# Kernel optimization log

Measured on AMD Instinct MI355X. Metric: run time of the kernel, lower is better.

The kernel has to match this reference:

```python
import jax, jax.numpy as jnp
import numpy as np
from jax import lax

N, CIN, H, W = 128, 1024, 14, 14
CF, TH = 128, 128          # cv_filter, te_hidden
HP, GT, FP, A = 256, 256, 256, 32


def setup_inputs() -> dict:
    key = jax.random.key(0)
    ks = jax.random.split(key, 12)
    s = 0.05
    return {
        "image": jax.random.normal(ks[0], (N, CIN, H, W), jnp.float32),
        "code": jax.random.normal(ks[1], (N, TH), jnp.float32),
        "conv_w": jax.random.normal(ks[2], (CF, CIN, 3, 3), jnp.float32) * 0.02,
        "conv_b": jnp.zeros((CF,), jnp.float32),
        "hp_w0": jax.random.normal(ks[3], (CF + 2 + TH, HP), jnp.float32) * s,
        "hp_b0": jnp.zeros((HP,), jnp.float32),
        "hp_w1": jax.random.normal(ks[4], (HP, 1), jnp.float32) * s,
        "hp_b1": jnp.zeros((1,), jnp.float32),
        "gt_w0": jax.random.normal(ks[5], ((CF + 2) * 2 + TH, GT), jnp.float32) * s,
        "gt_b0": jnp.zeros((GT,), jnp.float32),
        "gt_w1": jax.random.normal(ks[6], (GT, GT), jnp.float32) * s,
        "gt_b1": jnp.zeros((GT,), jnp.float32),
        "fp_w0": jax.random.normal(ks[7], (GT, FP), jnp.float32) * s,
        "fp_b0": jnp.zeros((FP,), jnp.float32),
        "fp_w1": jax.random.normal(ks[8], (FP, A), jnp.float32) * s,
        "fp_b1": jnp.zeros((A,), jnp.float32),
    }


def _sarn(image, code, conv_w, conv_b, hp_w0, hp_b0, hp_w1, hp_b1,
          gt_w0, gt_b0, gt_w1, gt_b1, fp_w0, fp_b0, fp_w1, fp_b1):
    # visual_resize: 3x3 conv, stride 1, pad 1 (NCHW)
    x = lax.conv_general_dilated(image, conv_w, (1, 1), "SAME",
                                 dimension_numbers=("NCHW", "OIHW", "NCHW"))
    x = x + conv_b[None, :, None, None]                       # [n, cf, h, w]
    n, c, h, w = x.shape
    o = h * w
    # sarn_encode: append x/y coordinate channels and question code
    xc = jnp.broadcast_to(jnp.linspace(-1.0, 1.0, h).reshape(1, 1, h, 1), (n, 1, h, w))
    yc = jnp.broadcast_to(jnp.linspace(-1.0, 1.0, w).reshape(1, 1, 1, w), (n, 1, h, w))
    coord = jnp.concatenate([x, xc, yc], axis=1)              # [n, cf+2, h, w]
    q = jnp.broadcast_to(code[:, :, None, None], (n, code.shape[1], h, w))
    qenc = jnp.concatenate([coord, q], axis=1)                # [n, cf+2+th, h, w]
    ce = coord.reshape(n, c + 2, o).transpose(0, 2, 1)        # [n, o, cf+2]
    qe = qenc.reshape(n, -1, o).transpose(0, 2, 1)            # [n, o, cf+2+th]
    # h_psi: per-object attention logit
    a = jax.nn.relu(jnp.einsum("nod,dh->noh", qe, hp_w0) + hp_b0)
    att = jnp.einsum("noh,hk->nok", a, hp_w1) + hp_b1         # [n, o, 1]
    # sarn_pair: softmax select a single soft object, pair with every object
    sel = jax.nn.softmax(att[..., 0], axis=1)                 # [n, o]
    selected = jnp.einsum("no,nod->nd", sel, ce)              # [n, cf+2]
    pairs = jnp.concatenate(
        [qe, jnp.broadcast_to(selected[:, None, :], ce.shape)], axis=2)  # [n, o, 2*(cf+2)+th]
    # g_theta MLP + sum over objects
    g = jax.nn.relu(jnp.einsum("nop,pg->nog", pairs, gt_w0) + gt_b0)
    g = jax.nn.relu(jnp.einsum("nog,gk->nok", g, gt_w1) + gt_b1)
    relations = g.sum(axis=1)                                 # [n, gt]
    # f_phi MLP -> answer logits
    f = jax.nn.relu(relations @ fp_w0 + fp_b0)
    return f @ fp_w1 + fp_b1                                  # [n, a_size]


def reference(image, code, conv_w, conv_b, hp_w0, hp_b0, hp_w1, hp_b1,
              gt_w0, gt_b0, gt_w1, gt_b1, fp_w0, fp_b0, fp_w1, fp_b1):
    return _sarn(image, code, conv_w, conv_b, hp_w0, hp_b0, hp_w1, hp_b1,
                 gt_w0, gt_b0, gt_w1, gt_b1, fp_w0, fp_b0, fp_w1, fp_b1)
```

## Files before the change

### kernel.cpp

```cpp
#include <hip/hip_runtime.h>
#include <stdint.h>

typedef unsigned short u16;
typedef __bf16 bf16x8 __attribute__((ext_vector_type(8)));
typedef float f32x4 __attribute__((ext_vector_type(4)));

__device__ __forceinline__ u16 f2b(float f) {
  union { float f; uint32_t u; } v; v.f = f;
  uint32_t r = v.u + 0x7fffu + ((v.u >> 16) & 1u);
  return (u16)(r >> 16);
}
__device__ __forceinline__ float b2f(u16 b) {
  union { float f; uint32_t u; } v; v.u = ((uint32_t)b) << 16;
  return v.f;
}
__device__ __forceinline__ void g2l16(const void* g, void* l) {
  __builtin_amdgcn_global_load_lds(
      (const __attribute__((address_space(1))) void*)g,
      (__attribute__((address_space(3))) void*)l, 16, 0, 0);
}

#define N_SAMP 128
#define OPAD   224
#define ROWS   (N_SAMP * OPAD)

__global__ __launch_bounds__(256) void prep_weights(
    const float* __restrict__ conv_w, const float* __restrict__ hp_w0,
    const float* __restrict__ gt_w0, const float* __restrict__ gt_w1,
    u16* __restrict__ W2, u16* __restrict__ hp_w0t,
    u16* __restrict__ gt_w0t, u16* __restrict__ gt_w1t) {
  int idx = blockIdx.x * 256 + threadIdx.x;
  const int nW2 = 9 * 128 * 1024;
  const int nHP = 256 * 288;
  const int nGT0 = 256 * 288;
  const int nGT1 = 256 * 256;
  if (idx < nW2) {
    int s = idx / 131072; int r = idx & 131071;
    int cf = r >> 10; int cin = r & 1023;
    W2[idx] = f2b(conv_w[(cf * 1024 + cin) * 9 + s]);
    return;
  }
  idx -= nW2;
  if (idx < nHP) {
    int nn = idx / 288, kk = idx % 288;
    hp_w0t[nn * 288 + kk] = (kk < 258) ? f2b(hp_w0[kk * 256 + nn]) : (u16)0;
    return;
  }
  idx -= nHP;
  if (idx < nGT0) {
    int nn = idx / 288, kk = idx % 288;
    gt_w0t[nn * 288 + kk] = (kk < 258) ? f2b(gt_w0[kk * 256 + nn]) : (u16)0;
    return;
  }
  idx -= nGT0;
  if (idx < nGT1) {
    int nn = idx >> 8, kk = idx & 255;
    gt_w1t[nn * 256 + kk] = f2b(gt_w1[kk * 256 + nn]);
  }
}

__global__ __launch_bounds__(256) void prep_img(const float* __restrict__ image,
                                                u16* __restrict__ imgT) {
  __shared__ float t[64][197];
  int n = blockIdx.x >> 4;
  int cin0 = (blockIdx.x & 15) * 64;
  const float* src = image + ((size_t)n * 1024 + cin0) * 196;
  for (int e = threadIdx.x; e < 64 * 196; e += 256) {
    int c = e / 196, sp = e % 196;
    t[c][sp] = src[c * 196 + sp];
  }
  __syncthreads();
  int w = threadIdx.x >> 6, lane = threadIdx.x & 63;
  for (int i = 0; i < 64; ++i) {
    int spg = i * 4 + w;
    int gy = spg >> 4, gx = spg & 15;
    float v = 0.f;
    if (gy >= 1 && gy <= 14 && gx >= 1 && gx <= 14) v = t[lane][(gy - 1) * 14 + (gx - 1)];
    imgT[(((size_t)(n * 256 + spg)) << 10) + cin0 + lane] = f2b(v);
  }
}

__global__ __launch_bounds__(256) void fill_qe(const float* __restrict__ code,
                                               u16* __restrict__ qeb) {
  int base = blockIdx.x * 8;
  for (int rr = 0; rr < 8; ++rr) {
    int r = base + rr;
    int n = r / 224, o = r % 224;
    int y = o / 14, x = o % 14;
    bool valid = o < 196;
    u16* row = qeb + (size_t)r * 288;
    for (int c = threadIdx.x; c < 288; c += 256) {
      u16 v;
      if (c < 128) { if (valid) continue; v = 0; }
      else if (c == 128) v = valid ? f2b(-1.f + 2.f * y / 13.f) : (u16)0;
      else if (c == 129) v = valid ? f2b(-1.f + 2.f * x / 13.f) : (u16)0;
      else if (c < 258) v = valid ? f2b(code[n * 128 + (c - 130)]) : (u16)0;
      else v = 0;
      row[c] = v;
    }
  }
}

__global__ __launch_bounds__(256) void conv_gemm(
    const u16* __restrict__ imgT, const u16* __restrict__ W2,
    const float* __restrict__ conv_b, u16* __restrict__ qeb) {
  __shared__ __align__(16) u16 lA[112 * 32];
  __shared__ __align__(16) u16 lB[128 * 32];
  int tid = threadIdx.x, lane = tid & 63, w = tid >> 6;
  int wg = blockIdx.x;
  int n = wg >> 1;
  int oBase = (wg & 1) * 112;
  int kb = (lane & 3) * 8;

  int oA0 = oBase + w * 16 + (lane >> 2);
  int oA1 = oBase + (w + 4) * 16 + (lane >> 2);
  int y0 = oA0 / 14, x0 = oA0 % 14; bool v0 = oA0 < 196;
  int y1 = oA1 / 14, x1 = oA1 % 14; bool v1 = oA1 < 196;
  bool has1 = (w < 3);

  int cf0 = w * 16 + (lane >> 2);
  int cf1 = (w + 4) * 16 + (lane >> 2);

  f32x4 acc[7][2];
#pragma unroll
  for (int mt = 0; mt < 7; ++mt)
#pragma unroll
    for (int j = 0; j < 2; ++j) acc[mt][j] = (f32x4){0.f, 0.f, 0.f, 0.f};

  int colW = w * 32;
  for (int s = 0; s < 9; ++s) {
    int dy = s / 3, dx = s % 3;
    int sp0 = v0 ? ((y0 + dy) * 16 + (x0 + dx)) : 0;
    int sp1 = v1 ? ((y1 + dy) * 16 + (x1 + dx)) : 0;
    const u16* gA0 = imgT + (((size_t)(n * 256 + sp0)) << 10) + kb;
    const u16* gA1 = imgT + (((size_t)(n * 256 + sp1)) << 10) + kb;
    const u16* gB0 = W2 + (((size_t)(s * 128 + cf0)) << 10) + kb;
    const u16* gB1 = W2 + (((size_t)(s * 128 + cf1)) << 10) + kb;
    for (int cb = 0; cb < 32; ++cb) {
      __syncthreads();
      g2l16(gA0 + cb * 32, &lA[w * 512]);
      if (has1) g2l16(gA1 + cb * 32, &lA[(w + 4) * 512]);
      g2l16(gB0 + cb * 32, &lB[w * 512]);
      g2l16(gB1 + cb * 32, &lB[(w + 4) * 512]);
      __syncthreads();
      bf16x8 af[7];
#pragma unroll
      for (int mt = 0; mt < 7; ++mt)
        af[mt] = *(const bf16x8*)&lA[(mt * 16 + (lane & 15)) * 32 + (lane >> 4) * 8];
#pragma unroll
      for (int j = 0; j < 2; ++j) {
        bf16x8 bfr = *(const bf16x8*)&lB[(colW + j * 16 + (lane & 15)) * 32 + (lane >> 4) * 8];
#pragma unroll
        for (int mt = 0; mt < 7; ++mt)
          acc[mt][j] = __builtin_amdgcn_mfma_f32_16x16x32_bf16(af[mt], bfr, acc[mt][j], 0, 0, 0);
      }
    }
  }
  int q = lane >> 4, c = lane & 15;
#pragma unroll
  for (int mt = 0; mt < 7; ++mt)
#pragma unroll
    for (int j = 0; j < 2; ++j) {
      int cf = colW + j * 16 + c;
      float bv = conv_b[cf];
#pragma unroll
      for (int r = 0; r < 4; ++r) {
        int o = oBase + mt * 16 + q * 4 + r;
        if (o < 196) qeb[(size_t)(n * 224 + o) * 288 + cf] = f2b(acc[mt][j][r] + bv);
      }
    }
}

template <int MODE, int KP, int KC>
__global__ __launch_bounds__(256) void gemm_kernel(
    const u16* __restrict__ A, const u16* __restrict__ Bt,
    const float* __restrict__ bias, const float* __restrict__ vec,
    float* __restrict__ outF, u16* __restrict__ outB) {
  __shared__ __align__(16) u16 lA[112 * 32];
  __shared__ __align__(16) u16 lB[128 * 32];
  int tid = threadIdx.x, lane = tid & 63, w = tid >> 6;
  int bx = blockIdx.x, by = blockIdx.y;
  int r0 = bx * 112;
  int cBase = by * 128;
  int kb = (lane & 3) * 8;
  int rA0 = r0 + w * 16 + (lane >> 2);
  int rA1 = r0 + (w + 4) * 16 + (lane >> 2);
  bool has1 = (w < 3);
  const u16* gA0 = A + (size_t)rA0 * KP + kb;
  const u16* gA1 = A + (size_t)rA1 * KP + kb;
  int cB0 = cBase + w * 16 + (lane >> 2);
  int cB1 = cBase + (w + 4) * 16 + (lane >> 2);
  const u16* gB0 = Bt + (size_t)cB0 * KP + kb;
  const u16* gB1 = Bt + (size_t)cB1 * KP + kb;

  f32x4 acc[7][2];
#pragma unroll
  for (int mt = 0; mt < 7; ++mt)
#pragma unroll
    for (int j = 0; j < 2; ++j) acc[mt][j] = (f32x4){0.f, 0.f, 0.f, 0.f};
  int colW = w * 32;

  for (int cb = 0; cb < KC; ++cb) {
    __syncthreads();
    g2l16(gA0 + cb * 32, &lA[w * 512]);
    if (has1) g2l16(gA1 + cb * 32, &lA[(w + 4) * 512]);
    g2l16(gB0 + cb * 32, &lB[w * 512]);
    g2l16(gB1 + cb * 32, &lB[(w + 4) * 512]);
    __syncthreads();
    bf16x8 af[7];
#pragma unroll
    for (int mt = 0; mt < 7; ++mt)
      af[mt] = *(const bf16x8*)&lA[(mt * 16 + (lane & 15)) * 32 + (lane >> 4) * 8];
#pragma unroll
    for (int j = 0; j < 2; ++j) {
      bf16x8 bfr = *(const bf16x8*)&lB[(colW + j * 16 + (lane & 15)) * 32 + (lane >> 4) * 8];
#pragma unroll
      for (int mt = 0; mt < 7; ++mt)
        acc[mt][j] = __builtin_amdgcn_mfma_f32_16x16x32_bf16(af[mt], bfr, acc[mt][j], 0, 0, 0);
    }
  }

  int q = lane >> 4, c = lane & 15;
  if (MODE == 0) {
    float attp[7][4];
#pragma unroll
    for (int mt = 0; mt < 7; ++mt)
#pragma unroll
      for (int r = 0; r < 4; ++r) attp[mt][r] = 0.f;
#pragma unroll
    for (int j = 0; j < 2; ++j) {
      int col = cBase + colW + j * 16 + c;
      float b0 = bias[col], w1 = vec[col];
#pragma unroll
      for (int mt = 0; mt < 7; ++mt)
#pragma unroll
        for (int r = 0; r < 4; ++r) {
          float v = fmaxf(acc[mt][j][r] + b0, 0.f);
          attp[mt][r] += v * w1;
        }
    }
#pragma unroll
    for (int mt = 0; mt < 7; ++mt)
#pragma unroll
      for (int r = 0; r < 4; ++r) {
        float p = attp[mt][r];
        p += __shfl_xor(p, 1, 64);
        p += __shfl_xor(p, 2, 64);
        p += __shfl_xor(p, 4, 64);
        p += __shfl_xor(p, 8, 64);
        if (c == 0) atomicAdd(&outF[r0 + mt * 16 + q * 4 + r], p);
      }
  } else if (MODE == 1) {
    int n = bx >> 1;
#pragma unroll
    for (int mt = 0; mt < 7; ++mt)
#pragma unroll
      for (int j = 0; j < 2; ++j) {
        int col = cBase + colW + j * 16 + c;
        float b = bias[n * 256 + col];
#pragma unroll
        for (int r = 0; r < 4; ++r) {
          int row = r0 + mt * 16 + q * 4 + r;
          outB[(size_t)row * 256 + col] = f2b(fmaxf(acc[mt][j][r] + b, 0.f));
        }
      }
  } else {
    int n = bx >> 1;
    int ob = (bx & 1) * 112;
#pragma unroll
    for (int j = 0; j < 2; ++j) {
      int col = cBase + colW + j * 16 + c;
      float b = bias[col];
      float sum = 0.f;
#pragma unroll
      for (int mt = 0; mt < 7; ++mt)
#pragma unroll
        for (int r = 0; r < 4; ++r) {
          int o = ob + mt * 16 + q * 4 + r;
          if (o < 196) sum += fmaxf(acc[mt][j][r] + b, 0.f);
        }
      sum += __shfl_xor(sum, 16, 64);
      sum += __shfl_xor(sum, 32, 64);
      if (q == 0) atomicAdd(&outF[n * 256 + col], sum);
    }
  }
}

__global__ __launch_bounds__(256) void sel_kernel(
    const float* __restrict__ att, const u16* __restrict__ qeb,
    const float* __restrict__ gt_w0, const float* __restrict__ gt_b0,
    float* __restrict__ bias2) {
  int n = blockIdx.x, t = threadIdx.x;
  __shared__ float sm[196];
  __shared__ float sel[130];
  __shared__ float red[8];
  float a = (t < 196) ? att[n * 224 + t] : -1e30f;
  float m = a;
  for (int mask = 1; mask < 64; mask <<= 1) m = fmaxf(m, __shfl_xor(m, mask, 64));
  if ((t & 63) == 0) red[t >> 6] = m;
  __syncthreads();
  float M = fmaxf(fmaxf(red[0], red[1]), fmaxf(red[2], red[3]));
  float e = (t < 196) ? expf(a - M) : 0.f;
  float sAcc = e;
  for (int mask = 1; mask < 64; mask <<= 1) sAcc += __shfl_xor(sAcc, mask, 64);
  if ((t & 63) == 0) red[4 + (t >> 6)] = sAcc;
  __syncthreads();
  float S = red[4] + red[5] + red[6] + red[7];
  if (t < 196) sm[t] = e / S;
  __syncthreads();
  if (t < 130) {
    float acc = 0.f;
    const u16* col = qeb + (size_t)n * 224 * 288 + t;
    for (int o = 0; o < 196; ++o) acc += sm[o] * b2f(col[(size_t)o * 288]);
    sel[t] = acc;
  }
  __syncthreads();
  float acc2 = gt_b0[t];
  for (int d = 0; d < 130; ++d) acc2 += sel[d] * gt_w0[(258 + d) * 256 + t];
  bias2[n * 256 + t] = acc2;
}

__global__ __launch_bounds__(256) void fphi(
    const float* __restrict__ relations, const float* __restrict__ fp_w0,
    const float* __restrict__ fp_b0, const float* __restrict__ fp_w1,
    const float* __restrict__ fp_b1, float* __restrict__ out) {
  int n = blockIdx.x, t = threadIdx.x;
  __shared__ float rel[256];
  __shared__ float f[256];
  rel[t] = relations[n * 256 + t];
  __syncthreads();
  float acc = fp_b0[t];
  for (int k = 0; k < 256; ++k) acc += rel[k] * fp_w0[k * 256 + t];
  f[t] = fmaxf(acc, 0.f);
  __syncthreads();
  if (t < 32) {
    float o = fp_b1[0];
    for (int k = 0; k < 256; ++k) o += f[k] * fp_w1[k * 32 + t];
    out[n * 32 + t] = o;
  }
}

extern "C" void kernel_launch(void* const* d_in, const int* in_sizes, int n_in,
                              void* d_out, int out_size, void* d_ws, size_t ws_size,
                              hipStream_t stream) {
  const float* image = (const float*)d_in[0];
  const float* code = (const float*)d_in[1];
  const float* conv_w = (const float*)d_in[2];
  const float* conv_b = (const float*)d_in[3];
  const float* hp_w0 = (const float*)d_in[4];
  const float* hp_b0 = (const float*)d_in[5];
  const float* hp_w1 = (const float*)d_in[6];
  const float* gt_w0 = (const float*)d_in[8];
  const float* gt_b0 = (const float*)d_in[9];
  const float* gt_w1 = (const float*)d_in[10];
  const float* gt_b1 = (const float*)d_in[11];
  const float* fp_w0 = (const float*)d_in[12];
  const float* fp_b0 = (const float*)d_in[13];
  const float* fp_w1 = (const float*)d_in[14];
  const float* fp_b1 = (const float*)d_in[15];
  float* out = (float*)d_out;

  char* p = (char*)d_ws;
  u16* imgT = (u16*)p;   p += (size_t)128 * 256 * 1024 * 2;
  u16* W2 = (u16*)p;     p += (size_t)9 * 128 * 1024 * 2;
  u16* qeb = (u16*)p;    p += (size_t)ROWS * 288 * 2;
  u16* hp_w0t = (u16*)p; p += (size_t)256 * 288 * 2;
  u16* gt_w0t = (u16*)p; p += (size_t)256 * 288 * 2;
  u16* gt_w1t = (u16*)p; p += (size_t)256 * 256 * 2;
  float* att = (float*)p;   p += (size_t)ROWS * 4;
  float* bias2 = (float*)p; p += (size_t)128 * 256 * 4;
  u16* g1 = (u16*)p;        p += (size_t)ROWS * 256 * 2;
  float* relations = (float*)p; p += (size_t)128 * 256 * 4;

  hipMemsetAsync(att, 0, (size_t)ROWS * 4, stream);
  hipMemsetAsync(relations, 0, (size_t)128 * 256 * 4, stream);

  prep_weights<<<5440, 256, 0, stream>>>(conv_w, hp_w0, gt_w0, gt_w1, W2, hp_w0t, gt_w0t, gt_w1t);
  prep_img<<<2048, 256, 0, stream>>>(image, imgT);
  fill_qe<<<ROWS / 8, 256, 0, stream>>>(code, qeb);
  conv_gemm<<<256, 256, 0, stream>>>(imgT, W2, conv_b, qeb);
  gemm_kernel<0, 288, 9><<<dim3(256, 2), 256, 0, stream>>>(qeb, hp_w0t, hp_b0, hp_w1, att, nullptr);
  sel_kernel<<<128, 256, 0, stream>>>(att, qeb, gt_w0, gt_b0, bias2);
  gemm_kernel<1, 288, 9><<<dim3(256, 2), 256, 0, stream>>>(qeb, gt_w0t, bias2, nullptr, nullptr, g1);
  gemm_kernel<2, 256, 8><<<dim3(256, 2), 256, 0, stream>>>(g1, gt_w1t, gt_b1, nullptr, relations, nullptr);
  fphi<<<128, 256, 0, stream>>>(relations, fp_w0, fp_b0, fp_w1, fp_b1, out);
}
```

Baseline: 459.1 us.

## Split conv GEMM over kernel rows with atomic reduction and swizzled LDS

The conv GEMM is split three ways along the 3x3 kernel taps, with 768 blocks in an XCD-aware ordering instead of 256. Partial sums are accumulated by fp32 atomics into a new buffer, and a separate conv_fix kernel adds the bias and writes bf16. The K-tile grows to 64, and XOR-swizzled LDS layouts are added to the conv and the generic GEMMs to avoid bank conflicts. sel_kernel now stages the qeb columns in shared memory before its strided reduction. The cost is an extra memset, extra atomics traffic and one more launch, with the g1 buffer aliased onto convAcc.

```diff
diff --git a/kernel.cpp b/kernel.cpp
--- a/kernel.cpp
+++ b/kernel.cpp
@@ -103,23 +103,28 @@
 
 __global__ __launch_bounds__(256) void conv_gemm(
     const u16* __restrict__ imgT, const u16* __restrict__ W2,
-    const float* __restrict__ conv_b, u16* __restrict__ qeb) {
-  __shared__ __align__(16) u16 lA[112 * 32];
-  __shared__ __align__(16) u16 lB[128 * 32];
+    float* __restrict__ convAcc) {
+  __shared__ __align__(16) u16 lA[112 * 64];
+  __shared__ __align__(16) u16 lB[128 * 64];
   int tid = threadIdx.x, lane = tid & 63, w = tid >> 6;
   int wg = blockIdx.x;
-  int n = wg >> 1;
-  int oBase = (wg & 1) * 112;
-  int kb = (lane & 3) * 8;
-
-  int oA0 = oBase + w * 16 + (lane >> 2);
-  int oA1 = oBase + (w + 4) * 16 + (lane >> 2);
-  int y0 = oA0 / 14, x0 = oA0 % 14; bool v0 = oA0 < 196;
-  int y1 = oA1 / 14, x1 = oA1 % 14; bool v1 = oA1 < 196;
-  bool has1 = (w < 3);
-
-  int cf0 = w * 16 + (lane >> 2);
-  int cf1 = (w + 4) * 16 + (lane >> 2);
+  int xcd = wg & 7, grp = wg >> 3;
+  int n = ((grp / 6) << 3) | xcd;
+  int r6 = grp % 6;
+  int oh = r6 / 3, ks = r6 % 3;
+  int oBase = oh * 112;
+  size_t nBase = (size_t)n << 8;
+  int rowIn = lane >> 3;
+  int cA = ((lane & 7) ^ rowIn) << 3;
+
+  int yxA[4];
+  for (int ii = 0; ii < 4; ++ii) {
+    int t = w + ii * 4;
+    int o = oBase + t * 8 + rowIn;
+    bool valid = o < 196;
+    int y = o / 14, x = o - y * 14;
+    yxA[ii] = valid ? (y * 16 + x) : 0;
+  }
 
   f32x4 acc[7][2];
 #pragma unroll
@@ -127,48 +132,70 @@
 #pragma unroll
     for (int j = 0; j < 2; ++j) acc[mt][j] = (f32x4){0.f, 0.f, 0.f, 0.f};
 
-  int colW = w * 32;
-  for (int s = 0; s < 9; ++s) {
-    int dy = s / 3, dx = s % 3;
-    int sp0 = v0 ? ((y0 + dy) * 16 + (x0 + dx)) : 0;
-    int sp1 = v1 ? ((y1 + dy) * 16 + (x1 + dx)) : 0;
-    const u16* gA0 = imgT + (((size_t)(n * 256 + sp0)) << 10) + kb;
-    const u16* gA1 = imgT + (((size_t)(n * 256 + sp1)) << 10) + kb;
-    const u16* gB0 = W2 + (((size_t)(s * 128 + cf0)) << 10) + kb;
-    const u16* gB1 = W2 + (((size_t)(s * 128 + cf1)) << 10) + kb;
-    for (int cb = 0; cb < 32; ++cb) {
+  int l = lane & 15, q = lane >> 4;
+  for (int si = 0; si < 3; ++si) {
+    int s = ks * 3 + si;
+    int off = (s / 3) * 16 + (s % 3);
+    const u16* Ws = W2 + ((size_t)(s * 128) << 10);
+    for (int cb = 0; cb < 16; ++cb) {
+      int k0 = cb << 6;
       __syncthreads();
-      g2l16(gA0 + cb * 32, &lA[w * 512]);
-      if (has1) g2l16(gA1 + cb * 32, &lA[(w + 4) * 512]);
-      g2l16(gB0 + cb * 32, &lB[w * 512]);
-      g2l16(gB1 + cb * 32, &lB[(w + 4) * 512]);
+      g2l16(imgT + ((nBase + (size_t)(yxA[0] + off)) << 10) + k0 + cA, &lA[(w) * 512]);
+      g2l16(imgT + ((nBase + (size_t)(yxA[1] + off)) << 10) + k0 + cA, &lA[(w + 4) * 512]);
+      g2l16(imgT + ((nBase + (size_t)(yxA[2] + off)) << 10) + k0 + cA, &lA[(w + 8) * 512]);
+      if (w < 2)
+        g2l16(imgT + ((nBase + (size_t)(yxA[3] + off)) << 10) + k0 + cA, &lA[(w + 12) * 512]);
+#pragma unroll
+      for (int ii = 0; ii < 4; ++ii) {
+        int t = w + ii * 4;
+        g2l16(Ws + ((size_t)(t * 8 + rowIn) << 10) + k0 + cA, &lB[t * 512]);
+      }
       __syncthreads();
-      bf16x8 af[7];
-#pragma unroll
-      for (int mt = 0; mt < 7; ++mt)
-        af[mt] = *(const bf16x8*)&lA[(mt * 16 + (lane & 15)) * 32 + (lane >> 4) * 8];
-#pragma unroll
-      for (int j = 0; j < 2; ++j) {
-        bf16x8 bfr = *(const bf16x8*)&lB[(colW + j * 16 + (lane & 15)) * 32 + (lane >> 4) * 8];
+#pragma unroll
+      for (int kk = 0; kk < 2; ++kk) {
+        int co = ((((kk << 2) | q) ^ (l & 7)) << 3);
+        bf16x8 af[7];
 #pragma unroll
         for (int mt = 0; mt < 7; ++mt)
-          acc[mt][j] = __builtin_amdgcn_mfma_f32_16x16x32_bf16(af[mt], bfr, acc[mt][j], 0, 0, 0);
+          af[mt] = *(const bf16x8*)&lA[(mt * 16 + l) * 64 + co];
+#pragma unroll
+        for (int jj = 0; jj < 2; ++jj) {
+          bf16x8 bb = *(const bf16x8*)&lB[(w * 32 + jj * 16 + l) * 64 + co];
+#pragma unroll
+          for (int mt = 0; mt < 7; ++mt)
+            acc[mt][jj] = __builtin_amdgcn_mfma_f32_16x16x32_bf16(af[mt], bb, acc[mt][jj], 0, 0, 0);
+        }
       }
     }
   }
-  int q = lane >> 4, c = lane & 15;
-#pragma unroll
-  for (int mt = 0; mt < 7; ++mt)
-#pragma unroll
-    for (int j = 0; j < 2; ++j) {
-      int cf = colW + j * 16 + c;
-      float bv = conv_b[cf];
-#pragma unroll
-      for (int r = 0; r < 4; ++r) {
-        int o = oBase + mt * 16 + q * 4 + r;
-        if (o < 196) qeb[(size_t)(n * 224 + o) * 288 + cf] = f2b(acc[mt][j][r] + bv);
+#pragma unroll
+  for (int mt = 0; mt < 7; ++mt) {
+    int o = oBase + mt * 16 + q * 4;
+#pragma unroll
+    for (int r4 = 0; r4 < 4; ++r4) {
+      if (o + r4 < 196) {
+        float* dst = convAcc + (size_t)(n * 224 + o + r4) * 128 + w * 32 + l;
+        atomicAdd(dst, acc[mt][0][r4]);
+        atomicAdd(dst + 16, acc[mt][1][r4]);
       }
     }
+  }
+}
+
+__global__ __launch_bounds__(256) void conv_fix(
+    const float* __restrict__ convAcc, const float* __restrict__ conv_b,
+    u16* __restrict__ qeb) {
+  int idx = blockIdx.x * 256 + threadIdx.x;
+  int row196 = idx >> 5;
+  int c0 = (idx & 31) << 2;
+  int n = row196 / 196, o = row196 - n * 196;
+  size_t row = (size_t)(n * 224 + o);
+  const float4 v = *(const float4*)(convAcc + (row << 7) + c0);
+  const float4 b = *(const float4*)(conv_b + c0);
+  ushort4 pk;
+  pk.x = f2b(v.x + b.x); pk.y = f2b(v.y + b.y);
+  pk.z = f2b(v.z + b.z); pk.w = f2b(v.w + b.w);
+  *(ushort4*)(qeb + row * 288 + c0) = pk;
 }
 
 template <int MODE, int KP, int KC>
@@ -182,7 +209,7 @@
   int bx = blockIdx.x, by = blockIdx.y;
   int r0 = bx * 112;
   int cBase = by * 128;
-  int kb = (lane & 3) * 8;
+  int kb = (((lane & 3) ^ ((lane >> 3) & 3)) << 3);
   int rA0 = r0 + w * 16 + (lane >> 2);
   int rA1 = r0 + (w + 4) * 16 + (lane >> 2);
   bool has1 = (w < 3);
@@ -199,6 +226,8 @@
 #pragma unroll
     for (int j = 0; j < 2; ++j) acc[mt][j] = (f32x4){0.f, 0.f, 0.f, 0.f};
   int colW = w * 32;
+  int l = lane & 15, q = lane >> 4;
+  int co = ((q ^ ((l >> 1) & 3)) << 3);
 
   for (int cb = 0; cb < KC; ++cb) {
     __syncthreads();
@@ -210,17 +239,17 @@
     bf16x8 af[7];
 #pragma unroll
     for (int mt = 0; mt < 7; ++mt)
-      af[mt] = *(const bf16x8*)&lA[(mt * 16 + (lane & 15)) * 32 + (lane >> 4) * 8];
+      af[mt] = *(const bf16x8*)&lA[(mt * 16 + l) * 32 + co];
 #pragma unroll
     for (int j = 0; j < 2; ++j) {
-      bf16x8 bfr = *(const bf16x8*)&lB[(colW + j * 16 + (lane & 15)) * 32 + (lane >> 4) * 8];
+      bf16x8 bfr = *(const bf16x8*)&lB[(colW + j * 16 + l) * 32 + co];
 #pragma unroll
       for (int mt = 0; mt < 7; ++mt)
         acc[mt][j] = __builtin_amdgcn_mfma_f32_16x16x32_bf16(af[mt], bfr, acc[mt][j], 0, 0, 0);
     }
   }
 
-  int q = lane >> 4, c = lane & 15;
+  int q4 = lane >> 4, c = lane & 15;
   if (MODE == 0) {
     float attp[7][4];
 #pragma unroll
@@ -248,7 +277,7 @@
         p += __shfl_xor(p, 2, 64);
         p += __shfl_xor(p, 4, 64);
         p += __shfl_xor(p, 8, 64);
-        if (c == 0) atomicAdd(&outF[r0 + mt * 16 + q * 4 + r], p);
+        if (c == 0) atomicAdd(&outF[r0 + mt * 16 + q4 * 4 + r], p);
       }
   } else if (MODE == 1) {
     int n = bx >> 1;
@@ -260,7 +289,7 @@
         float b = bias[n * 256 + col];
 #pragma unroll
         for (int r = 0; r < 4; ++r) {
-          int row = r0 + mt * 16 + q * 4 + r;
+          int row = r0 + mt * 16 + q4 * 4 + r;
           outB[(size_t)row * 256 + col] = f2b(fmaxf(acc[mt][j][r] + b, 0.f));
         }
       }
@@ -276,12 +305,12 @@
       for (int mt = 0; mt < 7; ++mt)
 #pragma unroll
         for (int r = 0; r < 4; ++r) {
-          int o = ob + mt * 16 + q * 4 + r;
+          int o = ob + mt * 16 + q4 * 4 + r;
           if (o < 196) sum += fmaxf(acc[mt][j][r] + b, 0.f);
         }
       sum += __shfl_xor(sum, 16, 64);
       sum += __shfl_xor(sum, 32, 64);
-      if (q == 0) atomicAdd(&outF[n * 256 + col], sum);
+      if (q4 == 0) atomicAdd(&outF[n * 256 + col], sum);
     }
   }
 }
@@ -291,27 +320,33 @@
     const float* __restrict__ gt_w0, const float* __restrict__ gt_b0,
     float* __restrict__ bias2) {
   int n = blockIdx.x, t = threadIdx.x;
+  int w = t >> 6, lane = t & 63;
+  __shared__ u16 sq[196][130];
   __shared__ float sm[196];
   __shared__ float sel[130];
   __shared__ float red[8];
+  const u16* base = qeb + (size_t)n * 224 * 288;
+  for (int o = w; o < 196; o += 4) {
+    const u16* rowp = base + (size_t)o * 288;
+    for (int c = lane; c < 130; c += 64) sq[o][c] = rowp[c];
+  }
   float a = (t < 196) ? att[n * 224 + t] : -1e30f;
   float m = a;
   for (int mask = 1; mask < 64; mask <<= 1) m = fmaxf(m, __shfl_xor(m, mask, 64));
-  if ((t & 63) == 0) red[t >> 6] = m;
+  if (lane == 0) red[w] = m;
   __syncthreads();
   float M = fmaxf(fmaxf(red[0], red[1]), fmaxf(red[2], red[3]));
   float e = (t < 196) ? expf(a - M) : 0.f;
   float sAcc = e;
   for (int mask = 1; mask < 64; mask <<= 1) sAcc += __shfl_xor(sAcc, mask, 64);
-  if ((t & 63) == 0) red[4 + (t >> 6)] = sAcc;
+  if (lane == 0) red[4 + w] = sAcc;
   __syncthreads();
   float S = red[4] + red[5] + red[6] + red[7];
   if (t < 196) sm[t] = e / S;
   __syncthreads();
   if (t < 130) {
     float acc = 0.f;
-    const u16* col = qeb + (size_t)n * 224 * 288 + t;
-    for (int o = 0; o < 196; ++o) acc += sm[o] * b2f(col[(size_t)o * 288]);
+    for (int o = 0; o < 196; ++o) acc += sm[o] * b2f(sq[o][t]);
     sel[t] = acc;
   }
   __syncthreads();
@@ -369,16 +404,19 @@
   u16* gt_w1t = (u16*)p; p += (size_t)256 * 256 * 2;
   float* att = (float*)p;   p += (size_t)ROWS * 4;
   float* bias2 = (float*)p; p += (size_t)128 * 256 * 4;
-  u16* g1 = (u16*)p;        p += (size_t)ROWS * 256 * 2;
+  float* convAcc = (float*)p; p += (size_t)ROWS * 128 * 4;
   float* relations = (float*)p; p += (size_t)128 * 256 * 4;
+  u16* g1 = (u16*)convAcc;
 
   hipMemsetAsync(att, 0, (size_t)ROWS * 4, stream);
   hipMemsetAsync(relations, 0, (size_t)128 * 256 * 4, stream);
+  hipMemsetAsync(convAcc, 0, (size_t)ROWS * 128 * 4, stream);
 
   prep_weights<<<5440, 256, 0, stream>>>(conv_w, hp_w0, gt_w0, gt_w1, W2, hp_w0t, gt_w0t, gt_w1t);
   prep_img<<<2048, 256, 0, stream>>>(image, imgT);
   fill_qe<<<ROWS / 8, 256, 0, stream>>>(code, qeb);
-  conv_gemm<<<256, 256, 0, stream>>>(imgT, W2, conv_b, qeb);
+  conv_gemm<<<768, 256, 0, stream>>>(imgT, W2, convAcc);
+  conv_fix<<<3136, 256, 0, stream>>>(convAcc, conv_b, qeb);
   gemm_kernel<0, 288, 9><<<dim3(256, 2), 256, 0, stream>>>(qeb, hp_w0t, hp_b0, hp_w1, att, nullptr);
   sel_kernel<<<128, 256, 0, stream>>>(att, qeb, gt_w0, gt_b0, bias2);
   gemm_kernel<1, 288, 9><<<dim3(256, 2), 256, 0, stream>>>(qeb, gt_w0t, bias2, nullptr, nullptr, g1);
```

Measured after the change: 412.9 us. 10.1% less time.
